# Kernel optimization log

Hardware: AMD Instinct MI355X
Metric: run time of the kernel (lower is better)

Reference implementation:

```python
import jax, jax.numpy as jnp
import numpy as np

B, T, D, N = 16, 512, 1024, 16


def setup_inputs() -> dict:
    key = jax.random.key(0)
    ks = jax.random.split(key, 6)
    x = jax.random.normal(ks[0], (B, T, D), dtype=jnp.float32)
    h_tape_init = jax.random.normal(ks[1], (B, N, D), dtype=jnp.float32) * 0.1
    h_work_init = jnp.zeros((B, D), dtype=jnp.float32)
    W_h = jax.random.normal(ks[2], (D, D), dtype=jnp.float32) * 0.02
    W_xz = jax.random.normal(ks[3], (2 * D, D), dtype=jnp.float32) * 0.02
    b_h = jnp.zeros((D,), dtype=jnp.float32)
    W_write = jax.random.normal(ks[4], (D, D), dtype=jnp.float32) * 0.02
    return {"x": x, "h_tape_init": h_tape_init, "h_work_init": h_work_init,
            "W_h": W_h, "W_xz": W_xz, "b_h": b_h, "W_write": W_write}


def _e29a_scan(x, h_tape_init, h_work_init, W_h, W_xz, b_h, W_write):
    d = W_h.shape[0]
    scale = 1.0 / (d ** 0.5)
    xz = jnp.einsum('btd,ed->bte', x, W_xz)          # [B,T,2D]
    x_proj = xz[:, :, :d]                             # [B,T,D]
    z = xz[:, :, d:]                                  # [B,T,D]

    def step(carry, inp):
        h_tape, h_work = carry                        # [B,N,D], [B,D]
        x_proj_t, z_t = inp                           # [B,D], [B,D]
        read_scores = jnp.einsum('bd,bnd->bn', h_work, h_tape) * scale
        read_attn = jax.nn.softmax(read_scores, axis=-1)
        read_val = jnp.einsum('bn,bnd->bd', read_attn, h_tape)
        h_work_new = jnp.tanh(x_proj_t + h_work @ W_h.T + read_val + b_h)
        write_val = h_work_new @ W_write.T            # [B,D]
        write_scores = jnp.einsum('bd,bnd->bn', write_val, h_tape) * scale
        write_attn = jax.nn.softmax(write_scores, axis=-1)
        wa = write_attn[:, :, None]                   # [B,N,1]
        h_tape_new = h_tape * (1.0 - wa) + write_val[:, None, :] * wa
        gate = jax.nn.silu(z_t + read_val + h_work_new)
        output = h_work_new * gate
        return (h_tape_new, h_work_new), output

    inputs = (jnp.swapaxes(x_proj, 0, 1), jnp.swapaxes(z, 0, 1))  # [T,B,D]
    (h_tape_final, _), out_t = jax.lax.scan(step, (h_tape_init, h_work_init), inputs)
    output_all = jnp.swapaxes(out_t, 0, 1)            # [B,T,D]
    return output_all, h_tape_final


def reference(x, h_tape_init, h_work_init, W_h, W_xz, b_h, W_write):
    return _e29a_scan(x, h_tape_init, h_work_init, W_h, W_xz, b_h, W_write)
```

## Files before the change

### kernel.cpp

```cpp
#include <hip/hip_runtime.h>

typedef _Float16 half8 __attribute__((ext_vector_type(8)));
typedef _Float16 half4_t __attribute__((ext_vector_type(4)));
typedef _Float16 half2_t __attribute__((ext_vector_type(2)));
typedef float f32x4 __attribute__((ext_vector_type(4)));
typedef float f32x2 __attribute__((ext_vector_type(2)));
typedef unsigned long long u64;
typedef unsigned int u32;

#define SCALE 0.03125f

#define XZ_OFF   0ULL
#define RING_OFF 33554432ULL
#define XBF_OFF  33554432ULL
#define WXZ_OFF  50331648ULL
#define WH_OFF   54525952ULL
#define WW_OFF   56623104ULL
#define VOTE_OFF 58720256ULL
#define SEN_OFF  58724352ULL

#define SLOTB 67584ULL
#define R_WVP 0
#define R_H   65536

union Pk2 { u64 u[2]; half8 h8; };

__device__ __forceinline__ float ldf(const float* p, bool mall) {
    return mall ? __hip_atomic_load(p, __ATOMIC_RELAXED, __HIP_MEMORY_SCOPE_AGENT) : *p;
}
__device__ __forceinline__ void stf(float* p, float v, bool mall) {
    if (mall) __hip_atomic_store(p, v, __ATOMIC_RELAXED, __HIP_MEMORY_SCOPE_AGENT); else *p = v;
}
__device__ __forceinline__ u64 ldq(const u64* p, bool mall) {
    return mall ? __hip_atomic_load(p, __ATOMIC_RELAXED, __HIP_MEMORY_SCOPE_AGENT) : *p;
}
__device__ __forceinline__ void stq(u64* p, u64 v, bool mall) {
    if (mall) __hip_atomic_store(p, v, __ATOMIC_RELAXED, __HIP_MEMORY_SCOPE_AGENT); else *p = v;
}
__device__ __forceinline__ u32 ldsen(u32* p, bool mall) {
    return mall ? __hip_atomic_load(p, __ATOMIC_RELAXED, __HIP_MEMORY_SCOPE_AGENT) : atomicAdd(p, 0u);
}
__device__ __forceinline__ void stsen(u32* p, u32 v, bool mall) {
    if (mall) __hip_atomic_store(p, v, __ATOMIC_RELAXED, __HIP_MEMORY_SCOPE_AGENT); else atomicExch(p, v);
}
__device__ __forceinline__ f32x4 ld4f(const float* p, bool mall) {
    if (mall) { f32x4 v; v[0]=ldf(p,1); v[1]=ldf(p+1,1); v[2]=ldf(p+2,1); v[3]=ldf(p+3,1); return v; }
    return *(const f32x4*)p;
}
__device__ __forceinline__ void st4f(float* p, f32x4 v, bool mall) {
    if (mall) { stf(p,v[0],1); stf(p+1,v[1],1); stf(p+2,v[2],1); stf(p+3,v[3],1); }
    else *(f32x4*)p = v;
}

#define FDOT(a,b,acc) acc = __builtin_amdgcn_fdot2((a),(b),(acc),false)
__device__ __forceinline__ half2_t hp2(half8 v, int i) {
    half2_t r; r[0] = v[2*i]; r[1] = v[2*i+1]; return r;
}

__global__ void cvt_kernel(const float* __restrict__ in, _Float16* __restrict__ o, int n4) {
    int i = blockIdx.x * 256 + threadIdx.x;
    if (i < n4) {
        f32x4 v = ((const f32x4*)in)[i];
        half4_t h;
        h[0] = (_Float16)v[0]; h[1] = (_Float16)v[1];
        h[2] = (_Float16)v[2]; h[3] = (_Float16)v[3];
        ((half4_t*)o)[i] = h;
    }
}

__launch_bounds__(256, 1)
__global__ void gemm_xz(const _Float16* __restrict__ A,
                        const _Float16* __restrict__ Bw,
                        _Float16* __restrict__ C) {
    __shared__ _Float16 As[128 * 40];
    __shared__ _Float16 Bs[128 * 40];
    const int tid = threadIdx.x;
    const int m0 = blockIdx.y * 128, n0 = blockIdx.x * 128;
    const int w = tid >> 6, lane = tid & 63;
    const int mw = (w >> 1) * 64, nw = (w & 1) * 64;
    const int row = lane & 15, q = lane >> 4;
    f32x4 acc[4][4];
    #pragma unroll
    for (int mt = 0; mt < 4; mt++)
        #pragma unroll
        for (int nt = 0; nt < 4; nt++)
            acc[mt][nt] = (f32x4){0.f, 0.f, 0.f, 0.f};

    for (int k0 = 0; k0 < 1024; k0 += 32) {
        __syncthreads();
        for (int cc = tid; cc < 512; cc += 256) {
            int r = cc >> 2, kc = (cc & 3) * 8;
            *(half8*)(&As[r * 40 + kc]) = *(const half8*)(&A[(size_t)(m0 + r) * 1024 + k0 + kc]);
            *(half8*)(&Bs[r * 40 + kc]) = *(const half8*)(&Bw[(size_t)(n0 + r) * 1024 + k0 + kc]);
        }
        __syncthreads();
        half8 af[4], bf[4];
        #pragma unroll
        for (int mt = 0; mt < 4; mt++) af[mt] = *(const half8*)(&As[(mw + mt * 16 + row) * 40 + q * 8]);
        #pragma unroll
        for (int nt = 0; nt < 4; nt++) bf[nt] = *(const half8*)(&Bs[(nw + nt * 16 + row) * 40 + q * 8]);
        #pragma unroll
        for (int mt = 0; mt < 4; mt++)
            #pragma unroll
            for (int nt = 0; nt < 4; nt++)
                acc[mt][nt] = __builtin_amdgcn_mfma_f32_16x16x32_f16(af[mt], bf[nt], acc[mt][nt], 0, 0, 0);
    }
    #pragma unroll
    for (int mt = 0; mt < 4; mt++)
        #pragma unroll
        for (int nt = 0; nt < 4; nt++)
            #pragma unroll
            for (int r = 0; r < 4; r++) {
                int gm = m0 + mw + mt * 16 + q * 4 + r;
                int gn = n0 + nw + nt * 16 + row;
                C[(size_t)gm * 2048 + gn] = (_Float16)acc[mt][nt][r];
            }
}

__launch_bounds__(256, 1)
__global__ void scan_kernel(const _Float16* __restrict__ xz,
                            const float* __restrict__ tape_in,
                            const float* __restrict__ h_in,
                            const float* __restrict__ bh,
                            const _Float16* __restrict__ wh,
                            const _Float16* __restrict__ ww,
                            char* ring,
                            u32* sen,
                            u32* vote,
                            float* __restrict__ out) {
    const int bx = blockIdx.x;
    const int g = (bx & 7) * 2 + ((bx >> 3) & 1);
    const int s = bx >> 4;
    const int tid = threadIdx.x;
    const int lane = tid & 63;
    const int cc = tid >> 2, q = tid & 3;
    const int nn = tid >> 4, c16 = tid & 15;

    __shared__ __align__(16) _Float16 h_prev[1024];
    __shared__ __align__(16) _Float16 h_own[64];
    __shared__ __align__(16) float rv_l[1024];
    __shared__ float p_l[256 * 17];
    __shared__ float sc_l[16];
    __shared__ float pad_l[15000];
    __shared__ int sh_same;

    { volatile float* vp = pad_l; vp[tid] = 0.f; }

    if (tid == 0) {
        u32 xcc;
        asm volatile("s_getreg_b32 %0, hwreg(HW_REG_XCC_ID)" : "=s"(xcc));
        xcc &= 7u;
        __hip_atomic_store(&vote[bx * 4], xcc + 1u, __ATOMIC_RELAXED, __HIP_MEMORY_SCOPE_AGENT);
        int same = 1; u32 ref = 0;
        for (int m = 0; m < 16; m++) {
            int mb = m * 16 + ((g & 1) << 3) + (g >> 1);
            u32 v; int spin = 0;
            while ((v = __hip_atomic_load(&vote[mb * 4], __ATOMIC_RELAXED, __HIP_MEMORY_SCOPE_AGENT)) == 0u) {
                if (++spin > 1000000) { v = 0xFFFFFFFFu; break; }
                __builtin_amdgcn_s_sleep(2);
            }
            if (m == 0) ref = v;
            if (v != ref || v == 0xFFFFFFFFu) same = 0;
        }
        sh_same = same;
    }
    __syncthreads();
    const bool mall = (sh_same == 0);
    bool dead = false;

    const int qx = q << 1;
    half8 whr[32];
    {
        const _Float16* wp = wh + (size_t)(s * 64 + cc) * 1024 + q * 256;
        #pragma unroll
        for (int jj = 0; jj < 32; jj++)
            whr[jj] = *(const half8*)(wp + ((jj ^ qx) * 8));
    }
    half8 wwr[4][8];
    {
        const _Float16* wp = ww + (size_t)(tid * 4) * 1024 + s * 64;
        #pragma unroll
        for (int jj = 0; jj < 4; jj++)
            #pragma unroll
            for (int kk = 0; kk < 8; kk++)
                wwr[jj][kk] = *(const half8*)(wp + jj * 1024 + kk * 8);
    }
    f32x4 tp[16];
    #pragma unroll
    for (int n = 0; n < 16; n++)
        tp[n] = *(const f32x4*)(&tape_in[(size_t)(g * 16 + n) * 1024 + tid * 4]);
    const float bhc = bh[s * 64 + cc];
    {
        f32x4 h4 = *(const f32x4*)(&h_in[(size_t)g * 1024 + tid * 4]);
        half4_t hh;
        hh[0] = (_Float16)h4[0]; hh[1] = (_Float16)h4[1];
        hh[2] = (_Float16)h4[2]; hh[3] = (_Float16)h4[3];
        *(half4_t*)(&h_prev[tid * 4]) = hh;
    }
    __syncthreads();

    u32* mysen = &sen[(g * 16 + s) * 32];
    const u32 senb = (u32)(g * 16);

    for (int t = 0; t <= 512; t++) {
        char* srd  = ring + (size_t)(g * 8 + ((t + 7) & 7)) * SLOTB;
        char* spub = ring + (size_t)(g * 8 + (t & 7)) * SLOTB;
        float xp = 0.f, zz = 0.f;
        if (t < 512) {
            size_t m = (size_t)(g * 512 + t) * 2048 + s * 64 + cc;
            xp = (float)xz[m];
            zz = (float)xz[m + 1024];
        }
        f32x4 wv4 = (f32x4){0.f, 0.f, 0.f, 0.f};
        if (t >= 1) {
            if (!dead && lane < 16) {
                int spin = 0;
                while (ldsen(&sen[(senb + lane) * 32], mall) < (u32)t) {
                    if (++spin > 2000000) { dead = true; break; }
                    __builtin_amdgcn_s_sleep(1);
                }
            }
            asm volatile("" ::: "memory");
            if (tid < 128) {
                const u64* Hp = (const u64*)(srd + R_H);
                Pk2 u;
                u.u[0] = ldq(&Hp[tid * 2], mall);
                u.u[1] = ldq(&Hp[tid * 2 + 1], mall);
                *(half8*)(&h_prev[tid * 8]) = u.h8;
            }
            const float* Wp = (const float*)(srd + R_WVP);
            #pragma unroll
            for (int sl = 0; sl < 16; sl++)
                wv4 += ld4f(&Wp[sl * 1024 + tid * 4], mall);
            {
                float p[16];
                #pragma unroll
                for (int n = 0; n < 16; n++) {
                    f32x4 d = tp[n];
                    p[n] = wv4[0]*d[0] + wv4[1]*d[1] + wv4[2]*d[2] + wv4[3]*d[3];
                }
                #pragma unroll
                for (int n = 0; n < 16; n++) p_l[tid * 17 + n] = p[n];
            }
            __syncthreads();
            {
                float scw = 0.f;
                #pragma unroll
                for (int m2 = 0; m2 < 16; m2++) scw += p_l[(c16 + 16 * m2) * 17 + nn];
                #pragma unroll
                for (int d2 = 1; d2 < 16; d2 <<= 1) scw += __shfl_xor(scw, d2, 16);
                if (c16 == 0) sc_l[nn] = scw;
            }
            __syncthreads();
            {
                float e[16], mxw = -1e30f;
                #pragma unroll
                for (int n = 0; n < 16; n++) { e[n] = sc_l[n] * SCALE; mxw = fmaxf(mxw, e[n]); }
                float smw = 0.f;
                #pragma unroll
                for (int n = 0; n < 16; n++) { e[n] = __expf(e[n] - mxw); smw += e[n]; }
                float invw = 1.f / smw;
                #pragma unroll
                for (int n = 0; n < 16; n++) {
                    float wan = e[n] * invw;
                    f32x4 d = tp[n];
                    d[0] += wan * (wv4[0] - d[0]);
                    d[1] += wan * (wv4[1] - d[1]);
                    d[2] += wan * (wv4[2] - d[2]);
                    d[3] += wan * (wv4[3] - d[3]);
                    tp[n] = d;
                }
            }
        }
        if (t == 512) break;

        {
            half4_t hh = *(const half4_t*)(&h_prev[tid * 4]);
            float h0 = (float)hh[0], h1 = (float)hh[1], h2 = (float)hh[2], h3 = (float)hh[3];
            float p[16];
            #pragma unroll
            for (int n = 0; n < 16; n++) {
                f32x4 d = tp[n];
                p[n] = h0*d[0] + h1*d[1] + h2*d[2] + h3*d[3];
            }
            #pragma unroll
            for (int n = 0; n < 16; n++) p_l[tid * 17 + n] = p[n];
        }
        __syncthreads();
        float sc = 0.f;
        #pragma unroll
        for (int m2 = 0; m2 < 16; m2++) sc += p_l[(c16 + 16 * m2) * 17 + nn];
        #pragma unroll
        for (int d2 = 1; d2 < 16; d2 <<= 1) sc += __shfl_xor(sc, d2, 16);
        if (c16 == 0) sc_l[nn] = sc;
        __syncthreads();
        float r[16], mx = -1e30f;
        #pragma unroll
        for (int n = 0; n < 16; n++) { r[n] = sc_l[n] * SCALE; mx = fmaxf(mx, r[n]); }
        float sm = 0.f;
        #pragma unroll
        for (int n = 0; n < 16; n++) { r[n] = __expf(r[n] - mx); sm += r[n]; }
        float inv = 1.f / sm;
        f32x4 rv4 = (f32x4){0.f, 0.f, 0.f, 0.f};
        #pragma unroll
        for (int n = 0; n < 16; n++) rv4 += (r[n] * inv) * tp[n];
        *(f32x4*)(&rv_l[tid * 4]) = rv4;
        float a0 = 0.f, a1 = 0.f, a2 = 0.f, a3 = 0.f;
        #pragma unroll
        for (int jj = 0; jj < 32; jj++) {
            half8 hp8 = *(const half8*)(&h_prev[q * 256 + ((jj ^ qx) * 8)]);
            half8 wc = whr[jj];
            FDOT(hp2(wc,0), hp2(hp8,0), a0);
            FDOT(hp2(wc,1), hp2(hp8,1), a1);
            FDOT(hp2(wc,2), hp2(hp8,2), a2);
            FDOT(hp2(wc,3), hp2(hp8,3), a3);
        }
        float av = (a0 + a1) + (a2 + a3);
        av += __shfl_xor(av, 1);
        av += __shfl_xor(av, 2);
        __syncthreads();
        float rd = rv_l[s * 64 + cc];
        float hv = tanhf(av + xp + rd + bhc);
        float g2 = zz + rd + hv;
        float o = hv * g2 / (1.f + __expf(-g2));
        if (q == 0) h_own[cc] = (_Float16)hv;
        __syncthreads();
        half8 hr[8];
        #pragma unroll
        for (int kk = 0; kk < 8; kk++) hr[kk] = *(const half8*)(&h_own[kk * 8]);
        float w0 = 0.f, w1 = 0.f, w2 = 0.f, w3 = 0.f;
        #pragma unroll
        for (int kk = 0; kk < 8; kk++) {
            half8 h8 = hr[kk];
            #pragma unroll
            for (int pp = 0; pp < 4; pp++) {
                FDOT(hp2(wwr[0][kk],pp), hp2(h8,pp), w0);
                FDOT(hp2(wwr[1][kk],pp), hp2(h8,pp), w1);
                FDOT(hp2(wwr[2][kk],pp), hp2(h8,pp), w2);
                FDOT(hp2(wwr[3][kk],pp), hp2(h8,pp), w3);
            }
        }
        {
            f32x4 wq; wq[0] = w0; wq[1] = w1; wq[2] = w2; wq[3] = w3;
            st4f((float*)(spub + R_WVP) + s * 1024 + tid * 4, wq, mall);
            if (tid < 8) {
                Pk2 u; u.h8 = *(const half8*)(&h_own[tid * 8]);
                u64* Hp = (u64*)(spub + R_H);
                stq(&Hp[s * 16 + tid * 2],     u.u[0], mall);
                stq(&Hp[s * 16 + tid * 2 + 1], u.u[1], mall);
            }
        }
        __syncthreads();
        if (tid == 0) stsen(mysen, (u32)(t + 1), mall);
        if (q == 0) out[(size_t)(g * 512 + t) * 1024 + s * 64 + cc] = o;
    }
    if (s == 0) {
        #pragma unroll
        for (int n = 0; n < 16; n++)
            *(f32x4*)(&out[8388608ULL + (size_t)(g * 16 + n) * 1024 + tid * 4]) = tp[n];
    }
}

extern "C" void kernel_launch(void* const* d_in, const int* in_sizes, int n_in,
                              void* d_out, int out_size, void* d_ws, size_t ws_size,
                              hipStream_t stream) {
    const float* x     = (const float*)d_in[0];
    const float* tape0 = (const float*)d_in[1];
    const float* h0    = (const float*)d_in[2];
    const float* Wh    = (const float*)d_in[3];
    const float* Wxz   = (const float*)d_in[4];
    const float* bh    = (const float*)d_in[5];
    const float* Ww    = (const float*)d_in[6];

    char* ws = (char*)d_ws;
    _Float16* xbf   = (_Float16*)(ws + XBF_OFF);
    _Float16* wxzbf = (_Float16*)(ws + WXZ_OFF);
    _Float16* whbf  = (_Float16*)(ws + WH_OFF);
    _Float16* wwbf  = (_Float16*)(ws + WW_OFF);
    _Float16* xzbf  = (_Float16*)(ws + XZ_OFF);
    char* ring      = ws + RING_OFF;
    u32* vote       = (u32*)(ws + VOTE_OFF);
    u32* sen        = (u32*)(ws + SEN_OFF);

    hipMemsetAsync(ws + VOTE_OFF, 0, 4096 + 32768, stream);

    cvt_kernel<<<8192, 256, 0, stream>>>(x, xbf, 2097152);
    cvt_kernel<<<2048, 256, 0, stream>>>(Wxz, wxzbf, 524288);
    cvt_kernel<<<1024, 256, 0, stream>>>(Wh, whbf, 262144);
    cvt_kernel<<<1024, 256, 0, stream>>>(Ww, wwbf, 262144);

    gemm_xz<<<dim3(16, 64), 256, 0, stream>>>(xbf, wxzbf, xzbf);

    scan_kernel<<<256, 256, 0, stream>>>(xzbf, tape0, h0, bh, whbf, wwbf,
                                         ring, sen, vote, (float*)d_out);
}
```

Measured before the change: 2.898 ms.

## Split h and write-val publication to overlap W_h matvec and read scores with write path

The kernel now publishes the new h with its own sentinel before computing the W_write matvec. Consumers can fetch h early and compute the W_h matvec and the read-score partials against the pre-update tape while the write values are still in flight. The read scores after the tape update are rebuilt algebraically from the pre-update scores, the write attention and an extra h·wv reduction, and the read value is formed without first applying the tape update. This shortens the critical path of the cross-block step dependency, at the cost of two sentinels per step, extra syncthreads and slightly different floating-point ordering.

```diff
diff --git a/kernel.cpp b/kernel.cpp
--- a/kernel.cpp
+++ b/kernel.cpp
@@ -132,15 +132,16 @@
     const int g = (bx & 7) * 2 + ((bx >> 3) & 1);
     const int s = bx >> 4;
     const int tid = threadIdx.x;
-    const int lane = tid & 63;
+    const int w = tid >> 6, lane = tid & 63;
     const int cc = tid >> 2, q = tid & 3;
     const int nn = tid >> 4, c16 = tid & 15;
 
     __shared__ __align__(16) _Float16 h_prev[1024];
     __shared__ __align__(16) _Float16 h_own[64];
     __shared__ __align__(16) float rv_l[1024];
-    __shared__ float p_l[256 * 17];
-    __shared__ float sc_l[16];
+    __shared__ float p_l[256 * 19];
+    __shared__ float sc_l[17];
+    __shared__ float q_sc[16];
     __shared__ float pad_l[15000];
     __shared__ int sh_same;
 
@@ -199,8 +200,47 @@
     }
     __syncthreads();
 
-    u32* mysen = &sen[(g * 16 + s) * 32];
-    const u32 senb = (u32)(g * 16);
+    u32* senrow = sen + (size_t)(g * 16 + s) * 32;
+    const int senb = g * 16;
+
+    float av;
+    {
+        float a0 = 0.f, a1 = 0.f, a2 = 0.f, a3 = 0.f;
+        #pragma unroll
+        for (int jj = 0; jj < 32; jj++) {
+            half8 hp8 = *(const half8*)(&h_prev[q * 256 + ((jj ^ qx) * 8)]);
+            half8 wc = whr[jj];
+            FDOT(hp2(wc,0), hp2(hp8,0), a0);
+            FDOT(hp2(wc,1), hp2(hp8,1), a1);
+            FDOT(hp2(wc,2), hp2(hp8,2), a2);
+            FDOT(hp2(wc,3), hp2(hp8,3), a3);
+        }
+        av = (a0 + a1) + (a2 + a3);
+        av += __shfl_xor(av, 1);
+        av += __shfl_xor(av, 2);
+    }
+    {
+        half4_t hh = *(const half4_t*)(&h_prev[tid * 4]);
+        float h0 = (float)hh[0], h1 = (float)hh[1], h2 = (float)hh[2], h3 = (float)hh[3];
+        #pragma unroll
+        for (int n = 0; n < 16; n++) {
+            f32x4 d = tp[n];
+            p_l[tid * 19 + n] = h0*d[0] + h1*d[1] + h2*d[2] + h3*d[3];
+        }
+    }
+    __syncthreads();
+    {
+        float sq = 0.f;
+        #pragma unroll
+        for (int m2 = 0; m2 < 16; m2++) sq += p_l[(c16 + 16 * m2) * 19 + nn];
+        #pragma unroll
+        for (int d2 = 1; d2 < 16; d2 <<= 1) sq += __shfl_xor(sq, d2, 16);
+        if (c16 == 0) q_sc[nn] = sq;
+    }
+    __syncthreads();
+
+    float wan[16];
+    f32x4 wv4 = (f32x4){0.f, 0.f, 0.f, 0.f};
 
     for (int t = 0; t <= 512; t++) {
         char* srd  = ring + (size_t)(g * 8 + ((t + 7) & 7)) * SLOTB;
@@ -211,45 +251,48 @@
             xp = (float)xz[m];
             zz = (float)xz[m + 1024];
         }
-        f32x4 wv4 = (f32x4){0.f, 0.f, 0.f, 0.f};
-        if (t >= 1) {
+        float hwv = 0.f;
+        const bool havew = (t >= 1);
+        if (havew) {
             if (!dead && lane < 16) {
                 int spin = 0;
-                while (ldsen(&sen[(senb + lane) * 32], mall) < (u32)t) {
+                while (ldsen(&sen[(size_t)(senb + lane) * 32 + 8], mall) < (u32)t) {
                     if (++spin > 2000000) { dead = true; break; }
                     __builtin_amdgcn_s_sleep(1);
                 }
             }
             asm volatile("" ::: "memory");
-            if (tid < 128) {
-                const u64* Hp = (const u64*)(srd + R_H);
-                Pk2 u;
-                u.u[0] = ldq(&Hp[tid * 2], mall);
-                u.u[1] = ldq(&Hp[tid * 2 + 1], mall);
-                *(half8*)(&h_prev[tid * 8]) = u.h8;
-            }
             const float* Wp = (const float*)(srd + R_WVP);
+            wv4 = (f32x4){0.f, 0.f, 0.f, 0.f};
             #pragma unroll
             for (int sl = 0; sl < 16; sl++)
                 wv4 += ld4f(&Wp[sl * 1024 + tid * 4], mall);
             {
-                float p[16];
+                half4_t hh = *(const half4_t*)(&h_prev[tid * 4]);
                 #pragma unroll
                 for (int n = 0; n < 16; n++) {
                     f32x4 d = tp[n];
-                    p[n] = wv4[0]*d[0] + wv4[1]*d[1] + wv4[2]*d[2] + wv4[3]*d[3];
-                }
-                #pragma unroll
-                for (int n = 0; n < 16; n++) p_l[tid * 17 + n] = p[n];
+                    p_l[tid * 19 + n] = wv4[0]*d[0] + wv4[1]*d[1] + wv4[2]*d[2] + wv4[3]*d[3];
+                }
+                p_l[tid * 19 + 16] = (float)hh[0]*wv4[0] + (float)hh[1]*wv4[1]
+                                   + (float)hh[2]*wv4[2] + (float)hh[3]*wv4[3];
             }
             __syncthreads();
             {
                 float scw = 0.f;
                 #pragma unroll
-                for (int m2 = 0; m2 < 16; m2++) scw += p_l[(c16 + 16 * m2) * 17 + nn];
+                for (int m2 = 0; m2 < 16; m2++) scw += p_l[(c16 + 16 * m2) * 19 + nn];
                 #pragma unroll
                 for (int d2 = 1; d2 < 16; d2 <<= 1) scw += __shfl_xor(scw, d2, 16);
                 if (c16 == 0) sc_l[nn] = scw;
+                if (nn == 0) {
+                    float hw = 0.f;
+                    #pragma unroll
+                    for (int m2 = 0; m2 < 16; m2++) hw += p_l[(c16 + 16 * m2) * 19 + 16];
+                    #pragma unroll
+                    for (int d2 = 1; d2 < 16; d2 <<= 1) hw += __shfl_xor(hw, d2, 16);
+                    if (c16 == 0) sc_l[16] = hw;
+                }
             }
             __syncthreads();
             {
@@ -261,63 +304,45 @@
                 for (int n = 0; n < 16; n++) { e[n] = __expf(e[n] - mxw); smw += e[n]; }
                 float invw = 1.f / smw;
                 #pragma unroll
-                for (int n = 0; n < 16; n++) {
-                    float wan = e[n] * invw;
-                    f32x4 d = tp[n];
-                    d[0] += wan * (wv4[0] - d[0]);
-                    d[1] += wan * (wv4[1] - d[1]);
-                    d[2] += wan * (wv4[2] - d[2]);
-                    d[3] += wan * (wv4[3] - d[3]);
-                    tp[n] = d;
-                }
-            }
-        }
-        if (t == 512) break;
-
-        {
-            half4_t hh = *(const half4_t*)(&h_prev[tid * 4]);
-            float h0 = (float)hh[0], h1 = (float)hh[1], h2 = (float)hh[2], h3 = (float)hh[3];
-            float p[16];
+                for (int n = 0; n < 16; n++) wan[n] = e[n] * invw;
+                hwv = sc_l[16];
+            }
+            if (t == 512) {
+                #pragma unroll
+                for (int n = 0; n < 16; n++) tp[n] += wan[n] * (wv4 - tp[n]);
+                break;
+            }
+        }
+        float r[16], mx = -1e30f;
+        if (havew) {
             #pragma unroll
             for (int n = 0; n < 16; n++) {
-                f32x4 d = tp[n];
-                p[n] = h0*d[0] + h1*d[1] + h2*d[2] + h3*d[3];
-            }
-            #pragma unroll
-            for (int n = 0; n < 16; n++) p_l[tid * 17 + n] = p[n];
-        }
-        __syncthreads();
-        float sc = 0.f;
-        #pragma unroll
-        for (int m2 = 0; m2 < 16; m2++) sc += p_l[(c16 + 16 * m2) * 17 + nn];
-        #pragma unroll
-        for (int d2 = 1; d2 < 16; d2 <<= 1) sc += __shfl_xor(sc, d2, 16);
-        if (c16 == 0) sc_l[nn] = sc;
-        __syncthreads();
-        float r[16], mx = -1e30f;
-        #pragma unroll
-        for (int n = 0; n < 16; n++) { r[n] = sc_l[n] * SCALE; mx = fmaxf(mx, r[n]); }
+                r[n] = ((1.f - wan[n]) * q_sc[n] + wan[n] * hwv) * SCALE;
+                mx = fmaxf(mx, r[n]);
+            }
+        } else {
+            #pragma unroll
+            for (int n = 0; n < 16; n++) { r[n] = q_sc[n] * SCALE; mx = fmaxf(mx, r[n]); }
+        }
         float sm = 0.f;
         #pragma unroll
         for (int n = 0; n < 16; n++) { r[n] = __expf(r[n] - mx); sm += r[n]; }
         float inv = 1.f / sm;
         f32x4 rv4 = (f32x4){0.f, 0.f, 0.f, 0.f};
-        #pragma unroll
-        for (int n = 0; n < 16; n++) rv4 += (r[n] * inv) * tp[n];
+        if (havew) {
+            float beta = 0.f;
+            #pragma unroll
+            for (int n = 0; n < 16; n++) {
+                float ran = r[n] * inv;
+                rv4 += (ran * (1.f - wan[n])) * tp[n];
+                beta += ran * wan[n];
+            }
+            rv4 += beta * wv4;
+        } else {
+            #pragma unroll
+            for (int n = 0; n < 16; n++) rv4 += (r[n] * inv) * tp[n];
+        }
         *(f32x4*)(&rv_l[tid * 4]) = rv4;
-        float a0 = 0.f, a1 = 0.f, a2 = 0.f, a3 = 0.f;
-        #pragma unroll
-        for (int jj = 0; jj < 32; jj++) {
-            half8 hp8 = *(const half8*)(&h_prev[q * 256 + ((jj ^ qx) * 8)]);
-            half8 wc = whr[jj];
-            FDOT(hp2(wc,0), hp2(hp8,0), a0);
-            FDOT(hp2(wc,1), hp2(hp8,1), a1);
-            FDOT(hp2(wc,2), hp2(hp8,2), a2);
-            FDOT(hp2(wc,3), hp2(hp8,3), a3);
-        }
-        float av = (a0 + a1) + (a2 + a3);
-        av += __shfl_xor(av, 1);
-        av += __shfl_xor(av, 2);
         __syncthreads();
         float rd = rv_l[s * 64 + cc];
         float hv = tanhf(av + xp + rd + bhc);
@@ -325,6 +350,16 @@
         float o = hv * g2 / (1.f + __expf(-g2));
         if (q == 0) h_own[cc] = (_Float16)hv;
         __syncthreads();
+        if (w == 0) {
+            if (tid < 8) {
+                Pk2 u; u.h8 = *(const half8*)(&h_own[tid * 8]);
+                u64* Hp = (u64*)(spub + R_H);
+                stq(&Hp[s * 16 + tid * 2],     u.u[0], mall);
+                stq(&Hp[s * 16 + tid * 2 + 1], u.u[1], mall);
+            }
+            asm volatile("s_waitcnt vmcnt(0)" ::: "memory");
+            if (tid == 0) stsen(&senrow[0], (u32)(t + 1), mall);
+        }
         half8 hr[8];
         #pragma unroll
         for (int kk = 0; kk < 8; kk++) hr[kk] = *(const half8*)(&h_own[kk * 8]);
@@ -343,16 +378,67 @@
         {
             f32x4 wq; wq[0] = w0; wq[1] = w1; wq[2] = w2; wq[3] = w3;
             st4f((float*)(spub + R_WVP) + s * 1024 + tid * 4, wq, mall);
-            if (tid < 8) {
-                Pk2 u; u.h8 = *(const half8*)(&h_own[tid * 8]);
-                u64* Hp = (u64*)(spub + R_H);
-                stq(&Hp[s * 16 + tid * 2],     u.u[0], mall);
-                stq(&Hp[s * 16 + tid * 2 + 1], u.u[1], mall);
-            }
         }
         __syncthreads();
-        if (tid == 0) stsen(mysen, (u32)(t + 1), mall);
+        if (tid == 0) stsen(&senrow[8], (u32)(t + 1), mall);
         if (q == 0) out[(size_t)(g * 512 + t) * 1024 + s * 64 + cc] = o;
+
+        if (havew) {
+            #pragma unroll
+            for (int n = 0; n < 16; n++) tp[n] += wan[n] * (wv4 - tp[n]);
+        }
+        if (t < 511) {
+            if (!dead && w < 2 && lane < 16) {
+                int spin = 0;
+                while (ldsen(&sen[(size_t)(senb + lane) * 32], mall) < (u32)(t + 1)) {
+                    if (++spin > 2000000) { dead = true; break; }
+                    __builtin_amdgcn_s_sleep(1);
+                }
+            }
+            asm volatile("" ::: "memory");
+            if (tid < 128) {
+                const u64* Hp = (const u64*)(spub + R_H);
+                Pk2 u;
+                u.u[0] = ldq(&Hp[tid * 2], mall);
+                u.u[1] = ldq(&Hp[tid * 2 + 1], mall);
+                *(half8*)(&h_prev[tid * 8]) = u.h8;
+            }
+            __syncthreads();
+            {
+                float a0 = 0.f, a1 = 0.f, a2 = 0.f, a3 = 0.f;
+                #pragma unroll
+                for (int jj = 0; jj < 32; jj++) {
+                    half8 hp8 = *(const half8*)(&h_prev[q * 256 + ((jj ^ qx) * 8)]);
+                    half8 wc = whr[jj];
+                    FDOT(hp2(wc,0), hp2(hp8,0), a0);
+                    FDOT(hp2(wc,1), hp2(hp8,1), a1);
+                    FDOT(hp2(wc,2), hp2(hp8,2), a2);
+                    FDOT(hp2(wc,3), hp2(hp8,3), a3);
+                }
+                av = (a0 + a1) + (a2 + a3);
+                av += __shfl_xor(av, 1);
+                av += __shfl_xor(av, 2);
+            }
+            {
+                half4_t hh = *(const half4_t*)(&h_prev[tid * 4]);
+                float h0 = (float)hh[0], h1 = (float)hh[1], h2 = (float)hh[2], h3 = (float)hh[3];
+                #pragma unroll
+                for (int n = 0; n < 16; n++) {
+                    f32x4 d = tp[n];
+                    p_l[tid * 19 + n] = h0*d[0] + h1*d[1] + h2*d[2] + h3*d[3];
+                }
+            }
+            __syncthreads();
+            {
+                float sq = 0.f;
+                #pragma unroll
+                for (int m2 = 0; m2 < 16; m2++) sq += p_l[(c16 + 16 * m2) * 19 + nn];
+                #pragma unroll
+                for (int d2 = 1; d2 < 16; d2 <<= 1) sq += __shfl_xor(sq, d2, 16);
+                if (c16 == 0) q_sc[nn] = sq;
+            }
+            __syncthreads();
+        }
     }
     if (s == 0) {
         #pragma unroll
```

Measured after the change: 3.719 ms. 28.3% more time.

## Fuse write and read attention reductions using algebraic tape-update identity, cutting barriers per step

Applied to the files above, without the earlier changes.

Read scores for step t are now computed against the old tape and corrected algebraically with the write attention and the h·write_val dot product, so the write-score and read-score reductions share one LDS pass and fewer __syncthreads. The tape update is deferred until after the read value is formed, and the epilogue (tanh, gate, output) is vectorized onto one 16-thread group per block. Sentinel loads and stores now always use relaxed atomics instead of atomicAdd/atomicExch. The aim is to shorten the serial per-step critical path, at the cost of a wider p_l scratch array and slightly different floating-point rounding.

```diff
diff --git a/kernel.cpp b/kernel.cpp
--- a/kernel.cpp
+++ b/kernel.cpp
@@ -24,6 +24,7 @@
 #define R_H   65536
 
 union Pk2 { u64 u[2]; half8 h8; };
+union Pk1 { u64 u; half4_t h; };
 
 __device__ __forceinline__ float ldf(const float* p, bool mall) {
     return mall ? __hip_atomic_load(p, __ATOMIC_RELAXED, __HIP_MEMORY_SCOPE_AGENT) : *p;
@@ -38,10 +39,10 @@
     if (mall) __hip_atomic_store(p, v, __ATOMIC_RELAXED, __HIP_MEMORY_SCOPE_AGENT); else *p = v;
 }
 __device__ __forceinline__ u32 ldsen(u32* p, bool mall) {
-    return mall ? __hip_atomic_load(p, __ATOMIC_RELAXED, __HIP_MEMORY_SCOPE_AGENT) : atomicAdd(p, 0u);
+    return __hip_atomic_load(p, __ATOMIC_RELAXED, __HIP_MEMORY_SCOPE_AGENT);
 }
 __device__ __forceinline__ void stsen(u32* p, u32 v, bool mall) {
-    if (mall) __hip_atomic_store(p, v, __ATOMIC_RELAXED, __HIP_MEMORY_SCOPE_AGENT); else atomicExch(p, v);
+    __hip_atomic_store(p, v, __ATOMIC_RELAXED, __HIP_MEMORY_SCOPE_AGENT);
 }
 __device__ __forceinline__ f32x4 ld4f(const float* p, bool mall) {
     if (mall) { f32x4 v; v[0]=ldf(p,1); v[1]=ldf(p+1,1); v[2]=ldf(p+2,1); v[3]=ldf(p+3,1); return v; }
@@ -133,15 +134,17 @@
     const int s = bx >> 4;
     const int tid = threadIdx.x;
     const int lane = tid & 63;
+    const int grp = tid >> 4, c16 = tid & 15;
     const int cc = tid >> 2, q = tid & 3;
-    const int nn = tid >> 4, c16 = tid & 15;
-
-    __shared__ __align__(16) _Float16 h_prev[1024];
+    const bool isEpi = (grp == s);
+    const int ep4 = c16 * 4;
+
+    __shared__ __align__(16) _Float16 h_l[1024];
     __shared__ __align__(16) _Float16 h_own[64];
-    __shared__ __align__(16) float rv_l[1024];
-    __shared__ float p_l[256 * 17];
-    __shared__ float sc_l[16];
-    __shared__ float pad_l[15000];
+    __shared__ float av_l[64];
+    __shared__ float p_l[256 * 35];
+    __shared__ float sc_l[33];
+    __shared__ float pad_l[11000];
     __shared__ int sh_same;
 
     { volatile float* vp = pad_l; vp[tid] = 0.f; }
@@ -189,141 +192,191 @@
     #pragma unroll
     for (int n = 0; n < 16; n++)
         tp[n] = *(const f32x4*)(&tape_in[(size_t)(g * 16 + n) * 1024 + tid * 4]);
-    const float bhc = bh[s * 64 + cc];
+    f32x4 bh4 = (f32x4){0.f, 0.f, 0.f, 0.f};
+    if (isEpi) bh4 = *(const f32x4*)(&bh[s * 64 + ep4]);
+
+    half4_t own4;
     {
         f32x4 h4 = *(const f32x4*)(&h_in[(size_t)g * 1024 + tid * 4]);
         half4_t hh;
         hh[0] = (_Float16)h4[0]; hh[1] = (_Float16)h4[1];
         hh[2] = (_Float16)h4[2]; hh[3] = (_Float16)h4[3];
-        *(half4_t*)(&h_prev[tid * 4]) = hh;
+        own4 = hh;
+        *(half4_t*)(&h_l[tid * 4]) = hh;
     }
     __syncthreads();
 
-    u32* mysen = &sen[(g * 16 + s) * 32];
-    const u32 senb = (u32)(g * 16);
+    u32* senrow = sen + (size_t)(g * 16 + s) * 32;
+    const int senb = g * 16;
+
+    float wan[16];
+    f32x4 wv4 = (f32x4){0.f, 0.f, 0.f, 0.f};
 
     for (int t = 0; t <= 512; t++) {
         char* srd  = ring + (size_t)(g * 8 + ((t + 7) & 7)) * SLOTB;
         char* spub = ring + (size_t)(g * 8 + (t & 7)) * SLOTB;
-        float xp = 0.f, zz = 0.f;
-        if (t < 512) {
-            size_t m = (size_t)(g * 512 + t) * 2048 + s * 64 + cc;
-            xp = (float)xz[m];
-            zz = (float)xz[m + 1024];
-        }
-        f32x4 wv4 = (f32x4){0.f, 0.f, 0.f, 0.f};
-        if (t >= 1) {
+        const bool havew = (t >= 1);
+        half4_t xp4h = (half4_t){(_Float16)0.f, (_Float16)0.f, (_Float16)0.f, (_Float16)0.f};
+        half4_t zz4h = xp4h;
+        if (isEpi && t < 512) {
+            size_t m = (size_t)(g * 512 + t) * 2048 + s * 64 + ep4;
+            xp4h = *(const half4_t*)(&xz[m]);
+            zz4h = *(const half4_t*)(&xz[m + 1024]);
+        }
+        if (havew) {
             if (!dead && lane < 16) {
                 int spin = 0;
-                while (ldsen(&sen[(senb + lane) * 32], mall) < (u32)t) {
+                while (ldsen(&sen[(size_t)(senb + lane) * 32], mall) < (u32)t) {
                     if (++spin > 2000000) { dead = true; break; }
                     __builtin_amdgcn_s_sleep(1);
                 }
             }
             asm volatile("" ::: "memory");
+            { Pk1 u; u.u = ldq(&((const u64*)(srd + R_H))[tid], mall); own4 = u.h; }
             if (tid < 128) {
                 const u64* Hp = (const u64*)(srd + R_H);
                 Pk2 u;
                 u.u[0] = ldq(&Hp[tid * 2], mall);
                 u.u[1] = ldq(&Hp[tid * 2 + 1], mall);
-                *(half8*)(&h_prev[tid * 8]) = u.h8;
+                *(half8*)(&h_l[tid * 8]) = u.h8;
             }
             const float* Wp = (const float*)(srd + R_WVP);
+            wv4 = (f32x4){0.f, 0.f, 0.f, 0.f};
             #pragma unroll
             for (int sl = 0; sl < 16; sl++)
                 wv4 += ld4f(&Wp[sl * 1024 + tid * 4], mall);
-            {
-                float p[16];
+        }
+        {
+            float h0 = (float)own4[0], h1 = (float)own4[1];
+            float h2 = (float)own4[2], h3 = (float)own4[3];
+            if (havew) {
                 #pragma unroll
                 for (int n = 0; n < 16; n++) {
                     f32x4 d = tp[n];
-                    p[n] = wv4[0]*d[0] + wv4[1]*d[1] + wv4[2]*d[2] + wv4[3]*d[3];
+                    p_l[tid * 35 + n] = wv4[0]*d[0] + wv4[1]*d[1] + wv4[2]*d[2] + wv4[3]*d[3];
                 }
-                #pragma unroll
-                for (int n = 0; n < 16; n++) p_l[tid * 17 + n] = p[n];
-            }
-            __syncthreads();
-            {
-                float scw = 0.f;
-                #pragma unroll
-                for (int m2 = 0; m2 < 16; m2++) scw += p_l[(c16 + 16 * m2) * 17 + nn];
-                #pragma unroll
-                for (int d2 = 1; d2 < 16; d2 <<= 1) scw += __shfl_xor(scw, d2, 16);
-                if (c16 == 0) sc_l[nn] = scw;
-            }
-            __syncthreads();
-            {
-                float e[16], mxw = -1e30f;
-                #pragma unroll
-                for (int n = 0; n < 16; n++) { e[n] = sc_l[n] * SCALE; mxw = fmaxf(mxw, e[n]); }
-                float smw = 0.f;
-                #pragma unroll
-                for (int n = 0; n < 16; n++) { e[n] = __expf(e[n] - mxw); smw += e[n]; }
-                float invw = 1.f / smw;
+                if (t < 512)
+                    p_l[tid * 35 + 32] = h0*wv4[0] + h1*wv4[1] + h2*wv4[2] + h3*wv4[3];
+            }
+            if (t < 512) {
                 #pragma unroll
                 for (int n = 0; n < 16; n++) {
-                    float wan = e[n] * invw;
                     f32x4 d = tp[n];
-                    d[0] += wan * (wv4[0] - d[0]);
-                    d[1] += wan * (wv4[1] - d[1]);
-                    d[2] += wan * (wv4[2] - d[2]);
-                    d[3] += wan * (wv4[3] - d[3]);
-                    tp[n] = d;
+                    p_l[tid * 35 + 16 + n] = h0*d[0] + h1*d[1] + h2*d[2] + h3*d[3];
                 }
             }
         }
-        if (t == 512) break;
-
-        {
-            half4_t hh = *(const half4_t*)(&h_prev[tid * 4]);
-            float h0 = (float)hh[0], h1 = (float)hh[1], h2 = (float)hh[2], h3 = (float)hh[3];
-            float p[16];
+        __syncthreads();
+        if (havew) {
+            float sw = 0.f;
+            #pragma unroll
+            for (int m2 = 0; m2 < 16; m2++) sw += p_l[(c16 + 16 * m2) * 35 + grp];
+            #pragma unroll
+            for (int d2 = 1; d2 < 16; d2 <<= 1) sw += __shfl_xor(sw, d2, 16);
+            if (c16 == 0) sc_l[grp] = sw;
+            if (grp == 0 && t < 512) {
+                float hw = 0.f;
+                #pragma unroll
+                for (int m2 = 0; m2 < 16; m2++) hw += p_l[(c16 + 16 * m2) * 35 + 32];
+                #pragma unroll
+                for (int d2 = 1; d2 < 16; d2 <<= 1) hw += __shfl_xor(hw, d2, 16);
+                if (c16 == 0) sc_l[32] = hw;
+            }
+        }
+        if (t < 512) {
+            float sq = 0.f;
+            #pragma unroll
+            for (int m2 = 0; m2 < 16; m2++) sq += p_l[(c16 + 16 * m2) * 35 + 16 + grp];
+            #pragma unroll
+            for (int d2 = 1; d2 < 16; d2 <<= 1) sq += __shfl_xor(sq, d2, 16);
+            if (c16 == 0) sc_l[16 + grp] = sq;
+            float a0 = 0.f, a1 = 0.f, a2 = 0.f, a3 = 0.f;
+            #pragma unroll
+            for (int jj = 0; jj < 32; jj++) {
+                half8 hp8 = *(const half8*)(&h_l[q * 256 + ((jj ^ qx) * 8)]);
+                half8 wc = whr[jj];
+                FDOT(hp2(wc,0), hp2(hp8,0), a0);
+                FDOT(hp2(wc,1), hp2(hp8,1), a1);
+                FDOT(hp2(wc,2), hp2(hp8,2), a2);
+                FDOT(hp2(wc,3), hp2(hp8,3), a3);
+            }
+            float av = (a0 + a1) + (a2 + a3);
+            av += __shfl_xor(av, 1);
+            av += __shfl_xor(av, 2);
+            if (q == 0) av_l[cc] = av;
+        }
+        __syncthreads();
+        float hwv = 0.f;
+        if (havew) {
+            float e[16], mxw = -1e30f;
+            #pragma unroll
+            for (int n = 0; n < 16; n++) { e[n] = sc_l[n] * SCALE; mxw = fmaxf(mxw, e[n]); }
+            float smw = 0.f;
+            #pragma unroll
+            for (int n = 0; n < 16; n++) { e[n] = __expf(e[n] - mxw); smw += e[n]; }
+            float invw = 1.f / smw;
+            #pragma unroll
+            for (int n = 0; n < 16; n++) wan[n] = e[n] * invw;
+            if (t < 512) hwv = sc_l[32];
+        }
+        if (t == 512) {
+            #pragma unroll
+            for (int n = 0; n < 16; n++) tp[n] += wan[n] * (wv4 - tp[n]);
+            break;
+        }
+        float r[16], mx = -1e30f;
+        if (havew) {
             #pragma unroll
             for (int n = 0; n < 16; n++) {
-                f32x4 d = tp[n];
-                p[n] = h0*d[0] + h1*d[1] + h2*d[2] + h3*d[3];
-            }
-            #pragma unroll
-            for (int n = 0; n < 16; n++) p_l[tid * 17 + n] = p[n];
-        }
-        __syncthreads();
-        float sc = 0.f;
-        #pragma unroll
-        for (int m2 = 0; m2 < 16; m2++) sc += p_l[(c16 + 16 * m2) * 17 + nn];
-        #pragma unroll
-        for (int d2 = 1; d2 < 16; d2 <<= 1) sc += __shfl_xor(sc, d2, 16);
-        if (c16 == 0) sc_l[nn] = sc;
-        __syncthreads();
-        float r[16], mx = -1e30f;
-        #pragma unroll
-        for (int n = 0; n < 16; n++) { r[n] = sc_l[n] * SCALE; mx = fmaxf(mx, r[n]); }
+                r[n] = ((1.f - wan[n]) * sc_l[16 + n] + wan[n] * hwv) * SCALE;
+                mx = fmaxf(mx, r[n]);
+            }
+        } else {
+            #pragma unroll
+            for (int n = 0; n < 16; n++) { r[n] = sc_l[16 + n] * SCALE; mx = fmaxf(mx, r[n]); }
+        }
         float sm = 0.f;
         #pragma unroll
         for (int n = 0; n < 16; n++) { r[n] = __expf(r[n] - mx); sm += r[n]; }
         float inv = 1.f / sm;
         f32x4 rv4 = (f32x4){0.f, 0.f, 0.f, 0.f};
-        #pragma unroll
-        for (int n = 0; n < 16; n++) rv4 += (r[n] * inv) * tp[n];
-        *(f32x4*)(&rv_l[tid * 4]) = rv4;
-        float a0 = 0.f, a1 = 0.f, a2 = 0.f, a3 = 0.f;
-        #pragma unroll
-        for (int jj = 0; jj < 32; jj++) {
-            half8 hp8 = *(const half8*)(&h_prev[q * 256 + ((jj ^ qx) * 8)]);
-            half8 wc = whr[jj];
-            FDOT(hp2(wc,0), hp2(hp8,0), a0);
-            FDOT(hp2(wc,1), hp2(hp8,1), a1);
-            FDOT(hp2(wc,2), hp2(hp8,2), a2);
-            FDOT(hp2(wc,3), hp2(hp8,3), a3);
-        }
-        float av = (a0 + a1) + (a2 + a3);
-        av += __shfl_xor(av, 1);
-        av += __shfl_xor(av, 2);
-        __syncthreads();
-        float rd = rv_l[s * 64 + cc];
-        float hv = tanhf(av + xp + rd + bhc);
-        float g2 = zz + rd + hv;
-        float o = hv * g2 / (1.f + __expf(-g2));
-        if (q == 0) h_own[cc] = (_Float16)hv;
+        if (havew) {
+            float beta = 0.f;
+            #pragma unroll
+            for (int n = 0; n < 16; n++) {
+                float ran = r[n] * inv;
+                rv4 += (ran * (1.f - wan[n])) * tp[n];
+                beta += ran * wan[n];
+            }
+            rv4 += beta * wv4;
+        } else {
+            #pragma unroll
+            for (int n = 0; n < 16; n++) rv4 += (r[n] * inv) * tp[n];
+        }
+        float o0 = 0.f, o1 = 0.f, o2 = 0.f, o3 = 0.f;
+        if (isEpi) {
+            f32x4 av4 = *(const f32x4*)(&av_l[ep4]);
+            float hv0 = tanhf(av4[0] + (float)xp4h[0] + rv4[0] + bh4[0]);
+            float hv1 = tanhf(av4[1] + (float)xp4h[1] + rv4[1] + bh4[1]);
+            float hv2 = tanhf(av4[2] + (float)xp4h[2] + rv4[2] + bh4[2]);
+            float hv3 = tanhf(av4[3] + (float)xp4h[3] + rv4[3] + bh4[3]);
+            float g0 = (float)zz4h[0] + rv4[0] + hv0;
+            float g1 = (float)zz4h[1] + rv4[1] + hv1;
+            float g2 = (float)zz4h[2] + rv4[2] + hv2;
+            float g3 = (float)zz4h[3] + rv4[3] + hv3;
+            o0 = hv0 * g0 / (1.f + __expf(-g0));
+            o1 = hv1 * g1 / (1.f + __expf(-g1));
+            o2 = hv2 * g2 / (1.f + __expf(-g2));
+            o3 = hv3 * g3 / (1.f + __expf(-g3));
+            half4_t hh;
+            hh[0] = (_Float16)hv0; hh[1] = (_Float16)hv1;
+            hh[2] = (_Float16)hv2; hh[3] = (_Float16)hv3;
+            *(half4_t*)(&h_own[ep4]) = hh;
+        }
+        if (havew) {
+            #pragma unroll
+            for (int n = 0; n < 16; n++) tp[n] += wan[n] * (wv4 - tp[n]);
+        }
         __syncthreads();
         half8 hr[8];
         #pragma unroll
@@ -343,16 +396,18 @@
         {
             f32x4 wq; wq[0] = w0; wq[1] = w1; wq[2] = w2; wq[3] = w3;
             st4f((float*)(spub + R_WVP) + s * 1024 + tid * 4, wq, mall);
-            if (tid < 8) {
-                Pk2 u; u.h8 = *(const half8*)(&h_own[tid * 8]);
-                u64* Hp = (u64*)(spub + R_H);
-                stq(&Hp[s * 16 + tid * 2],     u.u[0], mall);
-                stq(&Hp[s * 16 + tid * 2 + 1], u.u[1], mall);
-            }
-        }
-        __syncthreads();
-        if (tid == 0) stsen(mysen, (u32)(t + 1), mall);
-        if (q == 0) out[(size_t)(g * 512 + t) * 1024 + s * 64 + cc] = o;
+        }
+        if (tid < 8) {
+            Pk2 u; u.h8 = *(const half8*)(&h_own[tid * 8]);
+            u64* Hp = (u64*)(spub + R_H);
+            stq(&Hp[s * 16 + tid * 2],     u.u[0], mall);
+            stq(&Hp[s * 16 + tid * 2 + 1], u.u[1], mall);
+        }
+        __syncthreads();
+        if (tid == 0) stsen(&senrow[0], (u32)(t + 1), mall);
+        if (isEpi)
+            *(f32x4*)(&out[(size_t)(g * 512 + t) * 1024 + s * 64 + ep4]) =
+                (f32x4){o0, o1, o2, o3};
     }
     if (s == 0) {
         #pragma unroll
```

New measurement: 4.122 ms. 1.42x slower.

## Publish write partials in fp16 and sync via a shared atomic counter

Applied to the files above, without the earlier changes.

The per-step partial write vectors exchanged between the 16 blocks of a batch group are now stored as fp16 (one 8-byte store per thread instead of four 4-byte atomic stores), which halves the ring slot size and the cross-block traffic. The 16 per-block sentinel flags are replaced with a single per-group counter that each block atomically increments, and one lane polls it for 16*t instead of 16 lanes polling separate flags. This cuts inter-block communication latency on the sequential scan, at the cost of reduced precision in the summed write_val and added contention on one atomic counter.

```diff
diff --git a/kernel.cpp b/kernel.cpp
--- a/kernel.cpp
+++ b/kernel.cpp
@@ -19,37 +19,21 @@
 #define VOTE_OFF 58720256ULL
 #define SEN_OFF  58724352ULL
 
-#define SLOTB 67584ULL
+#define SLOTB 36864ULL
 #define R_WVP 0
-#define R_H   65536
+#define R_H   32768
 
 union Pk2 { u64 u[2]; half8 h8; };
-
-__device__ __forceinline__ float ldf(const float* p, bool mall) {
-    return mall ? __hip_atomic_load(p, __ATOMIC_RELAXED, __HIP_MEMORY_SCOPE_AGENT) : *p;
-}
-__device__ __forceinline__ void stf(float* p, float v, bool mall) {
-    if (mall) __hip_atomic_store(p, v, __ATOMIC_RELAXED, __HIP_MEMORY_SCOPE_AGENT); else *p = v;
-}
+union Pk1 { u64 u; half4_t h; };
+
 __device__ __forceinline__ u64 ldq(const u64* p, bool mall) {
     return mall ? __hip_atomic_load(p, __ATOMIC_RELAXED, __HIP_MEMORY_SCOPE_AGENT) : *p;
 }
 __device__ __forceinline__ void stq(u64* p, u64 v, bool mall) {
     if (mall) __hip_atomic_store(p, v, __ATOMIC_RELAXED, __HIP_MEMORY_SCOPE_AGENT); else *p = v;
 }
-__device__ __forceinline__ u32 ldsen(u32* p, bool mall) {
-    return mall ? __hip_atomic_load(p, __ATOMIC_RELAXED, __HIP_MEMORY_SCOPE_AGENT) : atomicAdd(p, 0u);
-}
-__device__ __forceinline__ void stsen(u32* p, u32 v, bool mall) {
-    if (mall) __hip_atomic_store(p, v, __ATOMIC_RELAXED, __HIP_MEMORY_SCOPE_AGENT); else atomicExch(p, v);
-}
-__device__ __forceinline__ f32x4 ld4f(const float* p, bool mall) {
-    if (mall) { f32x4 v; v[0]=ldf(p,1); v[1]=ldf(p+1,1); v[2]=ldf(p+2,1); v[3]=ldf(p+3,1); return v; }
-    return *(const f32x4*)p;
-}
-__device__ __forceinline__ void st4f(float* p, f32x4 v, bool mall) {
-    if (mall) { stf(p,v[0],1); stf(p+1,v[1],1); stf(p+2,v[2],1); stf(p+3,v[3],1); }
-    else *(f32x4*)p = v;
+__device__ __forceinline__ u32 ldsen(u32* p) {
+    return __hip_atomic_load(p, __ATOMIC_RELAXED, __HIP_MEMORY_SCOPE_AGENT);
 }
 
 #define FDOT(a,b,acc) acc = __builtin_amdgcn_fdot2((a),(b),(acc),false)
@@ -133,8 +117,8 @@
     const int s = bx >> 4;
     const int tid = threadIdx.x;
     const int lane = tid & 63;
+    const int nn = tid >> 4, c16 = tid & 15;
     const int cc = tid >> 2, q = tid & 3;
-    const int nn = tid >> 4, c16 = tid & 15;
 
     __shared__ __align__(16) _Float16 h_prev[1024];
     __shared__ __align__(16) _Float16 h_own[64];
@@ -190,6 +174,7 @@
     for (int n = 0; n < 16; n++)
         tp[n] = *(const f32x4*)(&tape_in[(size_t)(g * 16 + n) * 1024 + tid * 4]);
     const float bhc = bh[s * 64 + cc];
+
     {
         f32x4 h4 = *(const f32x4*)(&h_in[(size_t)g * 1024 + tid * 4]);
         half4_t hh;
@@ -199,12 +184,12 @@
     }
     __syncthreads();
 
-    u32* mysen = &sen[(g * 16 + s) * 32];
-    const u32 senb = (u32)(g * 16);
+    u32* cnt = sen + (size_t)g * 32;
 
     for (int t = 0; t <= 512; t++) {
         char* srd  = ring + (size_t)(g * 8 + ((t + 7) & 7)) * SLOTB;
         char* spub = ring + (size_t)(g * 8 + (t & 7)) * SLOTB;
+        const bool havew = (t >= 1);
         float xp = 0.f, zz = 0.f;
         if (t < 512) {
             size_t m = (size_t)(g * 512 + t) * 2048 + s * 64 + cc;
@@ -212,10 +197,10 @@
             zz = (float)xz[m + 1024];
         }
         f32x4 wv4 = (f32x4){0.f, 0.f, 0.f, 0.f};
-        if (t >= 1) {
-            if (!dead && lane < 16) {
+        if (havew) {
+            if (!dead && lane == 0) {
                 int spin = 0;
-                while (ldsen(&sen[(senb + lane) * 32], mall) < (u32)t) {
+                while (ldsen(cnt) < (u32)(16 * t)) {
                     if (++spin > 2000000) { dead = true; break; }
                     __builtin_amdgcn_s_sleep(1);
                 }
@@ -228,10 +213,13 @@
                 u.u[1] = ldq(&Hp[tid * 2 + 1], mall);
                 *(half8*)(&h_prev[tid * 8]) = u.h8;
             }
-            const float* Wp = (const float*)(srd + R_WVP);
-            #pragma unroll
-            for (int sl = 0; sl < 16; sl++)
-                wv4 += ld4f(&Wp[sl * 1024 + tid * 4], mall);
+            const u64* Wp = (const u64*)(srd + R_WVP);
+            #pragma unroll
+            for (int sl = 0; sl < 16; sl++) {
+                Pk1 u; u.u = ldq(&Wp[sl * 256 + tid], mall);
+                wv4[0] += (float)u.h[0]; wv4[1] += (float)u.h[1];
+                wv4[2] += (float)u.h[2]; wv4[3] += (float)u.h[3];
+            }
             {
                 float p[16];
                 #pragma unroll
@@ -341,8 +329,9 @@
             }
         }
         {
-            f32x4 wq; wq[0] = w0; wq[1] = w1; wq[2] = w2; wq[3] = w3;
-            st4f((float*)(spub + R_WVP) + s * 1024 + tid * 4, wq, mall);
+            Pk1 wq;
+            wq.h = (half4_t){(_Float16)w0, (_Float16)w1, (_Float16)w2, (_Float16)w3};
+            stq(&((u64*)(spub + R_WVP))[s * 256 + tid], wq.u, mall);
             if (tid < 8) {
                 Pk2 u; u.h8 = *(const half8*)(&h_own[tid * 8]);
                 u64* Hp = (u64*)(spub + R_H);
@@ -351,7 +340,8 @@
             }
         }
         __syncthreads();
-        if (tid == 0) stsen(mysen, (u32)(t + 1), mall);
+        if (tid == 0)
+            __hip_atomic_fetch_add(cnt, 1u, __ATOMIC_RELAXED, __HIP_MEMORY_SCOPE_AGENT);
         if (q == 0) out[(size_t)(g * 512 + t) * 1024 + s * 64 + cc] = o;
     }
     if (s == 0) {
```

After: 3.042 ms. 5.0% more time.
